# Performance work log

Hardware: AMD Instinct MI355X
Metric: run time of the kernel (lower is better)

## Reference

```python
import jax, jax.numpy as jnp
import numpy as np

N = 50000      # number of 'oa' nodes
E = 800000     # edges per metapath
IN_DIM = 128
OUT_DIM = 64   # per-head channels (concat=False -> mean over heads)
HEADS = 4
M = 3          # number of metapaths
NEG_SLOPE = 0.2  # PyG GATConv default leaky_relu slope


def setup_inputs() -> dict:
    key = jax.random.key(0)
    ks = jax.random.split(key, 32)
    inp = {"x": jax.random.normal(ks[0], (N, IN_DIM), jnp.float32)}
    for i in range(M):
        inp[f"edge_index_{i}"] = jax.random.randint(ks[1 + i], (2, E), 0, N, jnp.int32)
        inp[f"W_{i}"] = jax.random.normal(ks[4 + i], (IN_DIM, HEADS * OUT_DIM), jnp.float32) * (1.0 / np.sqrt(IN_DIM))
        inp[f"att_src_{i}"] = jax.random.normal(ks[7 + i], (HEADS, OUT_DIM), jnp.float32) * 0.1
        inp[f"att_dst_{i}"] = jax.random.normal(ks[10 + i], (HEADS, OUT_DIM), jnp.float32) * 0.1
        inp[f"bias_{i}"] = jnp.zeros((OUT_DIM,), jnp.float32)
    inp["proj_W"] = jax.random.normal(ks[20], (OUT_DIM, OUT_DIM), jnp.float32) * (1.0 / np.sqrt(OUT_DIM))
    inp["proj_b"] = jnp.zeros((OUT_DIM,), jnp.float32)
    inp["attn_vec"] = jax.random.normal(ks[21], (OUT_DIM,), jnp.float32) * 0.1
    return inp


def _gat_conv(x, edge_index, W, att_src, att_dst, bias):
    """PyG GATConv(in,out,heads,concat=False), eval mode, add_self_loops=True."""
    loop = jnp.arange(N, dtype=edge_index.dtype)
    src = jnp.concatenate([edge_index[0], loop])  # [E+N]
    dst = jnp.concatenate([edge_index[1], loop])
    h = (x @ W).reshape(N, HEADS, OUT_DIM)                 # [N,H,C]
    a_src = jnp.einsum('nhc,hc->nh', h, att_src)           # [N,H]
    a_dst = jnp.einsum('nhc,hc->nh', h, att_dst)
    e = jax.nn.leaky_relu(a_src[src] + a_dst[dst], NEG_SLOPE)  # [E+N,H]
    # edge softmax over incoming edges of each dst node (numerically stable)
    emax = jax.ops.segment_max(e, dst, num_segments=N)
    e = jnp.exp(e - emax[dst])
    denom = jax.ops.segment_sum(e, dst, num_segments=N)
    alpha = e / denom[dst]                                 # [E+N,H]; denom>0 via self loops
    out = jax.ops.segment_sum(h[src] * alpha[:, :, None], dst, num_segments=N)  # [N,H,C]
    return out.mean(axis=1) + bias                         # concat=False -> head mean


def reference(x, edge_index_0, edge_index_1, edge_index_2,
              W_0, W_1, W_2, att_src_0, att_src_1, att_src_2,
              att_dst_0, att_dst_1, att_dst_2, bias_0, bias_1, bias_2,
              proj_W, proj_b, attn_vec):
    eis = (edge_index_0, edge_index_1, edge_index_2)
    Ws = (W_0, W_1, W_2)
    a_s = (att_src_0, att_src_1, att_src_2)
    a_d = (att_dst_0, att_dst_1, att_dst_2)
    bs = (bias_0, bias_1, bias_2)
    z = [jax.nn.elu(_gat_conv(x, eis[i], Ws[i], a_s[i], a_d[i], bs[i])) for i in range(M)]
    z_stack = jnp.stack(z, axis=1)                          # [N,M,C]
    weights = jnp.tanh(z_stack @ proj_W + proj_b)           # [N,M,C]
    scores = jnp.einsum('nmc,c->nm', weights, attn_vec)     # [N,M]
    beta = jax.nn.softmax(scores, axis=1)                   # [N,M]
    z_final = jnp.einsum('nmc,nm->nc', z_stack, beta)       # [N,C]
    return z_final, beta
```

## Files before the change

kernel.cpp:

```cpp
#include <hip/hip_runtime.h>
#include <hip/hip_bf16.h>
#include <math.h>

#define NN 50000
#define EE 800000
#define IND 128
#define OUTD 64
#define NH 4
#define HC 256
#define WSZ 224
#define NWN 224
#define WCAP 4096
#define BATCH 2048
#define NBATCH ((EE + BATCH - 1) / BATCH)
#define PB (3 * NBATCH)
#define CVTB 6250
#define WPB 48
#define SORTB (3 * NWN)
#define NMT2 1563
#define MGB 391

typedef unsigned short u16;
typedef __attribute__((ext_vector_type(8))) short short8v;
typedef __attribute__((ext_vector_type(4))) float f32x4;
typedef __attribute__((ext_vector_type(2))) _Float16 half2v;

__device__ __forceinline__ float lrelu(float v) { return v > 0.f ? v : 0.2f * v; }
__device__ __forceinline__ u16 f2b(float f) {
  __hip_bfloat16 h = __float2bfloat16(f);
  return __builtin_bit_cast(u16, h);
}
__device__ __forceinline__ float b2f(u16 u) {
  return __uint_as_float((unsigned)u << 16);
}
__device__ __forceinline__ u16 f2h(float f) {
  _Float16 h = (_Float16)f;
  return __builtin_bit_cast(u16, h);
}
__device__ __forceinline__ float h2f(u16 u) {
  return (float)__builtin_bit_cast(_Float16, u);
}
__device__ __forceinline__ unsigned packh2(float a, float b) {
  half2v v = {(_Float16)a, (_Float16)b};
  return __builtin_bit_cast(unsigned, v);
}
__device__ __forceinline__ float dot2h(unsigned hpair, unsigned apair, float acc) {
#if __has_builtin(__builtin_amdgcn_fdot2)
  return __builtin_amdgcn_fdot2(__builtin_bit_cast(half2v, hpair),
                                __builtin_bit_cast(half2v, apair), acc, false);
#else
  acc = fmaf(h2f((u16)(hpair & 0xffff)), h2f((u16)(apair & 0xffff)), acc);
  return fmaf(h2f((u16)(hpair >> 16)), h2f((u16)(apair >> 16)), acc);
#endif
}

__global__ __launch_bounds__(256) void k_front(const int* __restrict__ ei0,
                                               const int* __restrict__ ei1,
                                               const int* __restrict__ ei2,
                                               int* __restrict__ gcur,
                                               unsigned int* __restrict__ glist,
                                               const float* __restrict__ x,
                                               u16* __restrict__ hi,
                                               u16* __restrict__ lo,
                                               const float* __restrict__ W0,
                                               const float* __restrict__ W1,
                                               const float* __restrict__ W2,
                                               const float* __restrict__ as0,
                                               const float* __restrict__ as1,
                                               const float* __restrict__ as2,
                                               const float* __restrict__ ad0,
                                               const float* __restrict__ ad1,
                                               const float* __restrict__ ad2,
                                               u16* __restrict__ wt,
                                               float* __restrict__ attS,
                                               float* __restrict__ attD) {
  __shared__ unsigned int stage[BATCH];
  __shared__ int cnt[NWN], strt[NWN], gbase[NWN];
  const int bx = blockIdx.x;
  const int tid = threadIdx.x;
  if (bx < PB) {
    const int m = bx / NBATCH;
    const int e0 = (bx - m * NBATCH) * BATCH;
    const int* ei = m == 0 ? ei0 : (m == 1 ? ei1 : ei2);
    if (tid < NWN) cnt[tid] = 0;
    __syncthreads();
    int bk[8], rk[8];
    unsigned int pk[8];
#pragma unroll
    for (int k = 0; k < 8; ++k) {
      const int e = e0 + k * 256 + tid;
      bk[k] = -1; rk[k] = 0; pk[k] = 0;
      if (e < EE) {
        const int d = ei[EE + e];
        const int s = ei[e];
        const int b = d / WSZ;
        bk[k] = b;
        pk[k] = ((unsigned)d << 16) | (unsigned)s;
        rk[k] = atomicAdd(&cnt[b], 1);
      }
    }
    __syncthreads();
    if (tid < 64) {
      const int base = tid * 4;
      int c0 = 0, c1 = 0, c2 = 0, c3 = 0;
      if (base + 0 < NWN) c0 = cnt[base + 0];
      if (base + 1 < NWN) c1 = cnt[base + 1];
      if (base + 2 < NWN) c2 = cnt[base + 2];
      if (base + 3 < NWN) c3 = cnt[base + 3];
      const int tot = c0 + c1 + c2 + c3;
      int run = tot;
#pragma unroll
      for (int off = 1; off < 64; off <<= 1) {
        const int u = __shfl_up(run, off, 64);
        if (tid >= off) run += u;
      }
      int ex = run - tot;
      if (base + 0 < NWN) { strt[base + 0] = ex; ex += c0; }
      if (base + 1 < NWN) { strt[base + 1] = ex; ex += c1; }
      if (base + 2 < NWN) { strt[base + 2] = ex; ex += c2; }
      if (base + 3 < NWN) { strt[base + 3] = ex; }
    }
    __syncthreads();
    if (tid < NWN && cnt[tid] > 0)
      gbase[tid] = atomicAdd(&gcur[m * NWN + tid], cnt[tid]);
#pragma unroll
    for (int k = 0; k < 8; ++k)
      if (bk[k] >= 0) stage[strt[bk[k]] + rk[k]] = pk[k];
    __syncthreads();
    const int unit = tid >> 3;
    const int l8 = tid & 7;
    for (int b = unit; b < NWN; b += 32) {
      const int len = cnt[b];
      if (len == 0) continue;
      const int st = strt[b];
      const int gb = gbase[b];
      unsigned int* dst = glist + (size_t)(m * NWN + b) * WCAP;
      for (int i = l8; i < len; i += 8)
        if (gb + i < WCAP) dst[gb + i] = stage[st + i];
    }
    return;
  }
  const int px = bx - PB;
  if (px < CVTB) {
    const int i = (px * 256 + tid) * 4;
    const float4 v = *(const float4*)(x + i);
    ushort4 h, l;
    h.x = f2b(v.x); l.x = f2b(v.x - b2f(h.x));
    h.y = f2b(v.y); l.y = f2b(v.y - b2f(h.y));
    h.z = f2b(v.z); l.z = f2b(v.z - b2f(h.z));
    h.w = f2b(v.w); l.w = f2b(v.w - b2f(h.w));
    *(ushort4*)(hi + i) = h;
    *(ushort4*)(lo + i) = l;
    return;
  }
  const int b = px - CVTB;
  const int m = b >> 4;
  const int kc = b & 15;
  const float* W = m == 0 ? W0 : (m == 1 ? W1 : W2);
  const int col = tid;
  const int colp = (col & 63) * 4 + (col >> 6);
#pragma unroll
  for (int kk = 0; kk < 8; ++kk) {
    const int k = kc * 8 + kk;
    wt[(size_t)m * (HC * IND) + colp * IND + k] = f2b(W[k * HC + col]);
  }
  if (kc == 0) {
    const float* as = m == 0 ? as0 : (m == 1 ? as1 : as2);
    const float* ad = m == 0 ? ad0 : (m == 1 ? ad1 : ad2);
    attS[m * HC + colp] = as[col];
    attD[m * HC + colp] = ad[col];
  }
}

__global__ __launch_bounds__(256) void k_mid(unsigned int* glist,
                                             const int* __restrict__ gcur,
                                             int* __restrict__ rowptr,
                                             const u16* __restrict__ xhi,
                                             const u16* __restrict__ xlo,
                                             const u16* __restrict__ wtB,
                                             const float* __restrict__ attSB,
                                             const float* __restrict__ attDB,
                                             u16* __restrict__ H16B,
                                             float* __restrict__ a_srcB,
                                             float* __restrict__ a_dstB,
                                             int nsort, int mbase,
                                             int strideH, int strideA) {
  __shared__ u16 srt[WCAP];
  __shared__ int cnt[WSZ], row[WSZ + 1], cur[WSZ];
  const int bx = blockIdx.x;
  const int tid = threadIdx.x;
  if (bx < nsort) {
    const int m = bx / NWN;
    const int w = bx - m * NWN;
    const int ne = min(gcur[m * NWN + w], WCAP);
    unsigned int* gl = glist + (size_t)(m * NWN + w) * WCAP;
    if (tid < WSZ) cnt[tid] = 0;
    __syncthreads();
    for (int i = tid; i < ne; i += 256)
      atomicAdd(&cnt[(int)(gl[i] >> 16) - w * WSZ], 1);
    __syncthreads();
    if (tid < 64) {
      const int base = tid * 4;
      int c0 = 0, c1 = 0, c2 = 0, c3 = 0;
      if (base + 0 < WSZ) c0 = cnt[base + 0];
      if (base + 1 < WSZ) c1 = cnt[base + 1];
      if (base + 2 < WSZ) c2 = cnt[base + 2];
      if (base + 3 < WSZ) c3 = cnt[base + 3];
      const int tot = c0 + c1 + c2 + c3;
      int run = tot;
#pragma unroll
      for (int off = 1; off < 64; off <<= 1) {
        const int u = __shfl_up(run, off, 64);
        if (tid >= off) run += u;
      }
      int ex = run - tot;
      if (base + 0 < WSZ) { row[base + 0] = ex; cur[base + 0] = ex; ex += c0; }
      if (base + 1 < WSZ) { row[base + 1] = ex; cur[base + 1] = ex; ex += c1; }
      if (base + 2 < WSZ) { row[base + 2] = ex; cur[base + 2] = ex; ex += c2; }
      if (base + 3 < WSZ) { row[base + 3] = ex; cur[base + 3] = ex; }
      if (tid == 63) row[WSZ] = ne;
    }
    __syncthreads();
    for (int i = tid; i < ne; i += 256) {
      const unsigned int v = gl[i];
      const int dl = (int)(v >> 16) - w * WSZ;
      const int p = atomicAdd(&cur[dl], 1);
      srt[p] = (u16)(v & 0xffffu);
    }
    __syncthreads();
    u16* cdst = (u16*)gl;
    for (int i = tid; i < ne; i += 256) cdst[i] = srt[i];
    int* rp = rowptr + (size_t)(m * NWN + w) * (WSZ + 1);
    if (tid <= WSZ) rp[tid] = row[tid];
    return;
  }
  const int b2 = bx - nsort;
  const int m = mbase + b2 / MGB;
  const int tg = b2 - (b2 / MGB) * MGB;
  const int wid = tid >> 6;
  const int l = tid & 63;
  const int l15 = l & 15;
  const int lq = l >> 4;
  const int mt = tg * 4 + wid;
  if (mt >= NMT2) return;
  const int m0 = mt * 32;
  const bool up = (m0 + 16 < NN);
  const u16* wt = wtB + (size_t)(m - mbase) * 0 + (size_t)m * (HC * IND);
  const float* attS = attSB + m * HC;
  const float* attD = attDB + m * HC;
  u16* H16 = H16B + (size_t)(m - mbase) * strideH;
  float* a_src = a_srcB + (size_t)(m - mbase) * strideA;
  float* a_dst = a_dstB + (size_t)(m - mbase) * strideA;
  const size_t aA = (size_t)(m0 + l15) * IND + lq * 8;
  const size_t aB = aA + (size_t)16 * IND;
  const u16* pb = wt + l15 * IND + lq * 8;
  f32x4 accA[16], accB[16];
#pragma unroll
  for (int nt = 0; nt < 16; ++nt) {
    accA[nt] = (f32x4){0.f, 0.f, 0.f, 0.f};
    accB[nt] = (f32x4){0.f, 0.f, 0.f, 0.f};
  }
#pragma unroll
  for (int ks = 0; ks < 4; ++ks) {
    const short8v a0h = *(const short8v*)(xhi + aA + ks * 32);
    const short8v a0l = *(const short8v*)(xlo + aA + ks * 32);
    short8v a1h = (short8v){0,0,0,0,0,0,0,0};
    short8v a1l = (short8v){0,0,0,0,0,0,0,0};
    if (up) {
      a1h = *(const short8v*)(xhi + aB + ks * 32);
      a1l = *(const short8v*)(xlo + aB + ks * 32);
    }
#pragma unroll
    for (int nt = 0; nt < 16; ++nt) {
      const short8v b0 = *(const short8v*)(pb + nt * 16 * IND + ks * 32);
      accA[nt] = __builtin_amdgcn_mfma_f32_16x16x32_bf16(a0h, b0, accA[nt], 0, 0, 0);
      accA[nt] = __builtin_amdgcn_mfma_f32_16x16x32_bf16(a0l, b0, accA[nt], 0, 0, 0);
      accB[nt] = __builtin_amdgcn_mfma_f32_16x16x32_bf16(a1h, b0, accB[nt], 0, 0, 0);
      accB[nt] = __builtin_amdgcn_mfma_f32_16x16x32_bf16(a1l, b0, accB[nt], 0, 0, 0);
    }
  }
#pragma unroll
  for (int nt = 0; nt < 16; ++nt) {
#pragma unroll
    for (int r = 0; r < 4; ++r)
      H16[(size_t)(m0 + lq * 4 + r) * HC + nt * 16 + l15] = f2h(accA[nt][r]);
  }
  if (up) {
#pragma unroll
    for (int nt = 0; nt < 16; ++nt) {
#pragma unroll
      for (int r = 0; r < 4; ++r)
        H16[(size_t)(m0 + 16 + lq * 4 + r) * HC + nt * 16 + l15] = f2h(accB[nt][r]);
    }
  }
  float asv[16], adv[16];
#pragma unroll
  for (int nt = 0; nt < 16; ++nt) {
    asv[nt] = attS[nt * 16 + l15];
    adv[nt] = attD[nt * 16 + l15];
  }
#pragma unroll
  for (int r = 0; r < 4; ++r) {
    float ps = 0.f, pd = 0.f, ps2 = 0.f, pd2 = 0.f;
#pragma unroll
    for (int nt = 0; nt < 16; ++nt) {
      ps = fmaf(accA[nt][r], asv[nt], ps);
      pd = fmaf(accA[nt][r], adv[nt], pd);
      ps2 = fmaf(accB[nt][r], asv[nt], ps2);
      pd2 = fmaf(accB[nt][r], adv[nt], pd2);
    }
    ps += __shfl_xor(ps, 4, 64); ps += __shfl_xor(ps, 8, 64);
    pd += __shfl_xor(pd, 4, 64); pd += __shfl_xor(pd, 8, 64);
    ps2 += __shfl_xor(ps2, 4, 64); ps2 += __shfl_xor(ps2, 8, 64);
    pd2 += __shfl_xor(pd2, 4, 64); pd2 += __shfl_xor(pd2, 8, 64);
    if (l15 < 4) {
      const int n = m0 + lq * 4 + r;
      a_src[n * NH + l15] = ps;
      a_dst[n * NH + l15] = pd;
      if (up) {
        a_src[(n + 16) * NH + l15] = ps2;
        a_dst[(n + 16) * NH + l15] = pd2;
      }
    }
  }
}

__global__ __launch_bounds__(256) void k_aggr(const unsigned int* __restrict__ glistB,
                                              const int* __restrict__ rowptrB,
                                              const u16* __restrict__ H16B,
                                              const float* __restrict__ a_srcB,
                                              const float* __restrict__ a_dstB,
                                              const float* __restrict__ b0_,
                                              const float* __restrict__ b1_,
                                              const float* __restrict__ b2_,
                                              u16* __restrict__ zbB,
                                              int mbase, int strideH, int strideA) {
  __shared__ uint4 slot[4][64];
  const int m = mbase + blockIdx.y;
  const unsigned int* glist_m = glistB + (size_t)m * NWN * WCAP;
  const int* rowptrm = rowptrB + (size_t)m * NWN * (WSZ + 1);
  const u16* H16 = H16B + (size_t)blockIdx.y * strideH;
  const float* a_src = a_srcB + (size_t)blockIdx.y * strideA;
  const float* a_dst = a_dstB + (size_t)blockIdx.y * strideA;
  const float* bias = m == 0 ? b0_ : (m == 1 ? b1_ : b2_);
  u16* zb = zbB + (size_t)m * NN * OUTD;
  const int wid = threadIdx.x >> 6;
  const int c = threadIdx.x & 63;
  const int d = blockIdx.x * 4 + wid;
  const int w = d / WSZ;
  const int dl = d - w * WSZ;
  const int* rp = rowptrm + (size_t)w * (WSZ + 1);
  const int r0 = rp[dl];
  const int nb = min(rp[dl + 1] - r0, 64);
  const u16* cw = (const u16*)(glist_m + (size_t)w * WCAP);
  const float4 adv = *(const float4*)&a_dst[d * NH];
  float4 evr = make_float4(0.f, 0.f, 0.f, 0.f);
  int sj = 0;
  if (c < nb) {
    sj = cw[r0 + c];
    const float4 asv = *(const float4*)&a_src[sj * NH];
    evr.x = __expf(lrelu(asv.x + adv.x));
    evr.y = __expf(lrelu(asv.y + adv.y));
    evr.z = __expf(lrelu(asv.z + adv.z));
    evr.w = __expf(lrelu(asv.w + adv.w));
  }
  float den0 = evr.x, den1 = evr.y, den2 = evr.z, den3 = evr.w;
#pragma unroll
  for (int mk = 32; mk; mk >>= 1) {
    den0 += __shfl_xor(den0, mk, 64);
    den1 += __shfl_xor(den1, mk, 64);
    den2 += __shfl_xor(den2, mk, 64);
    den3 += __shfl_xor(den3, mk, 64);
  }
  const float4 asl = *(const float4*)&a_src[d * NH];
  const float e0s = __expf(lrelu(asl.x + adv.x));
  const float e1s = __expf(lrelu(asl.y + adv.y));
  const float e2s = __expf(lrelu(asl.z + adv.z));
  const float e3s = __expf(lrelu(asl.w + adv.w));
  den0 += e0s; den1 += e1s; den2 += e2s; den3 += e3s;
  const float rd0 = 0.25f * __builtin_amdgcn_rcpf(den0);
  const float rd1 = 0.25f * __builtin_amdgcn_rcpf(den1);
  const float rd2 = 0.25f * __builtin_amdgcn_rcpf(den2);
  const float rd3 = 0.25f * __builtin_amdgcn_rcpf(den3);
  if (c < nb) {
    uint4 sv;
    sv.x = packh2(evr.x * rd0, evr.y * rd1);
    sv.y = packh2(evr.z * rd2, evr.w * rd3);
    sv.z = (unsigned)(sj * (HC * 2));
    sv.w = 0;
    slot[wid][c] = sv;
  }
  const ushort4 hs = *(const ushort4*)&H16[(size_t)d * HC + c * 4];
  float res = e0s * rd0 * h2f(hs.x);
  res = fmaf(e1s * rd1, h2f(hs.y), res);
  res = fmaf(e2s * rd2, h2f(hs.z), res);
  res = fmaf(e3s * rd3, h2f(hs.w), res);
  const unsigned char* Hb = (const unsigned char*)H16;
  const int c8 = c * 8;
  float accA = 0.f, accB = 0.f, accC = 0.f, accD = 0.f;
  int j = 0;
  for (; j + 4 <= nb; j += 4) {
    const uint4 sa = slot[wid][j + 0];
    const uint4 sb = slot[wid][j + 1];
    const uint4 sc = slot[wid][j + 2];
    const uint4 sd = slot[wid][j + 3];
    const uint2 ha = *(const uint2*)(Hb + (size_t)sa.z + c8);
    const uint2 hb = *(const uint2*)(Hb + (size_t)sb.z + c8);
    const uint2 hc = *(const uint2*)(Hb + (size_t)sc.z + c8);
    const uint2 hd = *(const uint2*)(Hb + (size_t)sd.z + c8);
    accA = dot2h(ha.x, sa.x, accA); accA = dot2h(ha.y, sa.y, accA);
    accB = dot2h(hb.x, sb.x, accB); accB = dot2h(hb.y, sb.y, accB);
    accC = dot2h(hc.x, sc.x, accC); accC = dot2h(hc.y, sc.y, accC);
    accD = dot2h(hd.x, sd.x, accD); accD = dot2h(hd.y, sd.y, accD);
  }
  for (; j < nb; ++j) {
    const uint4 sa = slot[wid][j];
    const uint2 ha = *(const uint2*)(Hb + (size_t)sa.z + c8);
    accA = dot2h(ha.x, sa.x, accA);
    accA = dot2h(ha.y, sa.y, accA);
  }
  res += (accA + accB) + (accC + accD);
  res += bias[c];
  res = res > 0.f ? res : __expf(res) - 1.f;
  zb[(size_t)d * OUTD + c] = f2b(res);
}

__global__ __launch_bounds__(256) void k_sem(const u16* __restrict__ zb,
                                             const float* __restrict__ proj_W,
                                             const float* __restrict__ proj_b,
                                             const float* __restrict__ attn_vec,
                                             float* __restrict__ out) {
  __shared__ float zl[3][16][OUTD];
  const int tid = threadIdx.x;
  const int n0 = blockIdx.x * 16;
  const int wid = tid >> 6;
  const int c = tid & 63;
  float pwc[64];
#pragma unroll
  for (int k = 0; k < 64; ++k) pwc[k] = proj_W[k * OUTD + c];
#pragma unroll
  for (int mm = 0; mm < 3; ++mm) {
    const ushort4 v = ((const ushort4*)(zb + ((size_t)mm * NN + n0) * OUTD))[tid];
    float4 f;
    f.x = b2f(v.x); f.y = b2f(v.y); f.z = b2f(v.z); f.w = b2f(v.w);
    *(float4*)&zl[mm][tid >> 4][(tid & 15) * 4] = f;
  }
  __syncthreads();
  const float pb = proj_b[c];
  const float av = attn_vec[c];
  for (int nl = 0; nl < 4; ++nl) {
    const int node = wid * 4 + nl;
    float s[3];
#pragma unroll
    for (int mm = 0; mm < 3; ++mm) {
      const float4* zr = (const float4*)&zl[mm][node][0];
      float a0 = pb, a1 = 0.f, a2 = 0.f, a3 = 0.f;
#pragma unroll
      for (int kq = 0; kq < 4; ++kq) {
        const float4 z0 = zr[kq * 4 + 0];
        const float4 z1 = zr[kq * 4 + 1];
        const float4 z2 = zr[kq * 4 + 2];
        const float4 z3 = zr[kq * 4 + 3];
        a0 = fmaf(z0.x, pwc[kq * 16 + 0], a0);
        a0 = fmaf(z0.y, pwc[kq * 16 + 1], a0);
        a0 = fmaf(z0.z, pwc[kq * 16 + 2], a0);
        a0 = fmaf(z0.w, pwc[kq * 16 + 3], a0);
        a1 = fmaf(z1.x, pwc[kq * 16 + 4], a1);
        a1 = fmaf(z1.y, pwc[kq * 16 + 5], a1);
        a1 = fmaf(z1.z, pwc[kq * 16 + 6], a1);
        a1 = fmaf(z1.w, pwc[kq * 16 + 7], a1);
        a2 = fmaf(z2.x, pwc[kq * 16 + 8], a2);
        a2 = fmaf(z2.y, pwc[kq * 16 + 9], a2);
        a2 = fmaf(z2.z, pwc[kq * 16 + 10], a2);
        a2 = fmaf(z2.w, pwc[kq * 16 + 11], a2);
        a3 = fmaf(z3.x, pwc[kq * 16 + 12], a3);
        a3 = fmaf(z3.y, pwc[kq * 16 + 13], a3);
        a3 = fmaf(z3.z, pwc[kq * 16 + 14], a3);
        a3 = fmaf(z3.w, pwc[kq * 16 + 15], a3);
      }
      float xx = (a0 + a1) + (a2 + a3);
      xx = fminf(xx, 40.f);
      const float t = __expf(2.f * xx);
      const float th = (t - 1.f) * __builtin_amdgcn_rcpf(t + 1.f);
      float p = th * av;
#pragma unroll
      for (int mk = 32; mk; mk >>= 1) p += __shfl_xor(p, mk, 64);
      s[mm] = p;
    }
    const float mx = fmaxf(s[0], fmaxf(s[1], s[2]));
    const float e0 = __expf(s[0] - mx), e1 = __expf(s[1] - mx), e2 = __expf(s[2] - mx);
    const float inv = 1.0f / (e0 + e1 + e2);
    const float b0 = e0 * inv, b1 = e1 * inv, b2 = e2 * inv;
    const int n = n0 + node;
    const float zf = zl[0][node][c] * b0 + zl[1][node][c] * b1 + zl[2][node][c] * b2;
    out[(size_t)n * OUTD + c] = zf;
    if (c < 3) out[(size_t)NN * OUTD + n * 3 + c] = (c == 0 ? b0 : (c == 1 ? b1 : b2));
  }
}

extern "C" void kernel_launch(void* const* d_in, const int* in_sizes, int n_in,
                              void* d_out, int out_size, void* d_ws, size_t ws_size,
                              hipStream_t stream) {
  const float* x = (const float*)d_in[0];
  const int* ei[3];
  const float* W[3];
  const float* as[3];
  const float* ad[3];
  const float* bs[3];

  if (in_sizes[2] != 2 * EE) {
    for (int m = 0; m < 3; ++m) {
      ei[m] = (const int*)d_in[1 + 5 * m];
      W[m]  = (const float*)d_in[2 + 5 * m];
      as[m] = (const float*)d_in[3 + 5 * m];
      ad[m] = (const float*)d_in[4 + 5 * m];
      bs[m] = (const float*)d_in[5 + 5 * m];
    }
  } else {
    for (int m = 0; m < 3; ++m) {
      ei[m] = (const int*)d_in[1 + m];
      W[m]  = (const float*)d_in[4 + m];
      as[m] = (const float*)d_in[7 + m];
      ad[m] = (const float*)d_in[10 + m];
      bs[m] = (const float*)d_in[13 + m];
    }
  }
  const float* proj_W = (const float*)d_in[16];
  const float* proj_b = (const float*)d_in[17];
  const float* attn_vec = (const float*)d_in[18];

  const bool batched = (ws_size >= (size_t)139000000);
  const int nrep = batched ? 3 : 1;

  char* ws = (char*)d_ws;
  size_t off = 0;
  u16* x16hi = (u16*)(ws + off);                     off += (size_t)NN * IND * 2;
  u16* x16lo = (u16*)(ws + off);                     off += (size_t)NN * IND * 2;
  u16* H16 = (u16*)(ws + off);                       off += (size_t)nrep * NN * HC * 2;
  u16* zb = (u16*)(ws + off);                        off += (size_t)3 * NN * OUTD * 2;
  float* a_srcb = (float*)(ws + off);                off += (size_t)nrep * NN * NH * 4;
  float* a_dstb = (float*)(ws + off);                off += (size_t)nrep * NN * NH * 4;
  int* gcur = (int*)(ws + off);                      off += (size_t)3 * NWN * 4;
  unsigned int* glist = (unsigned int*)(ws + off);   off += (size_t)3 * NWN * WCAP * 4;
  int* rowptr = (int*)(ws + off);                    off += (size_t)3 * NWN * (WSZ + 1) * 4;
  u16* wt16 = (u16*)(ws + off);                      off += (size_t)3 * HC * IND * 2;
  float* attSp = (float*)(ws + off);                 off += (size_t)3 * HC * 4;
  float* attDp = (float*)(ws + off);                 off += (size_t)3 * HC * 4;

  float* outp = (float*)d_out;

  hipMemsetAsync(gcur, 0, (size_t)3 * NWN * sizeof(int), stream);
  k_front<<<PB + CVTB + WPB, 256, 0, stream>>>(ei[0], ei[1], ei[2], gcur, glist,
                                               x, x16hi, x16lo,
                                               W[0], W[1], W[2], as[0], as[1], as[2],
                                               ad[0], ad[1], ad[2], wt16, attSp, attDp);

  if (batched) {
    k_mid<<<SORTB + 3 * MGB, 256, 0, stream>>>(glist, gcur, rowptr,
                                               x16hi, x16lo, wt16, attSp, attDp,
                                               H16, a_srcb, a_dstb,
                                               SORTB, 0, NN * HC, NN * NH);
    k_aggr<<<dim3(NN / 4, 3), 256, 0, stream>>>(
        glist, rowptr, H16, a_srcb, a_dstb, bs[0], bs[1], bs[2], zb,
        0, NN * HC, NN * NH);
  } else {
    k_mid<<<SORTB + MGB, 256, 0, stream>>>(glist, gcur, rowptr,
                                           x16hi, x16lo, wt16, attSp, attDp,
                                           H16, a_srcb, a_dstb,
                                           SORTB, 0, 0, 0);
    k_aggr<<<dim3(NN / 4, 1), 256, 0, stream>>>(
        glist, rowptr, H16, a_srcb, a_dstb, bs[0], bs[1], bs[2], zb, 0, 0, 0);
    for (int m = 1; m < 3; ++m) {
      k_mid<<<MGB, 256, 0, stream>>>(glist, gcur, rowptr,
                                     x16hi, x16lo, wt16, attSp, attDp,
                                     H16, a_srcb, a_dstb,
                                     0, m, 0, 0);
      k_aggr<<<dim3(NN / 4, 1), 256, 0, stream>>>(
          glist, rowptr, H16, a_srcb, a_dstb, bs[0], bs[1], bs[2], zb, m, 0, 0);
    }
  }
  k_sem<<<NN / 16, 256, 0, stream>>>(zb, proj_W, proj_b, attn_vec, outp);
}
```

Baseline: 320.1 us.

## Fuse x bf16 split into GEMM, loop metapaths per wave, double edge batch

The separate pass that split x into bf16 hi/lo arrays in the front kernel is removed. The GEMM kernel now reads fp32 x directly, converts it in registers once, and reuses those fragments across all metapaths. Each wave now handles a 16-row tile and loops over the 3 metapaths instead of a 32-row tile for one metapath, which cuts x reads and the hi/lo workspace traffic. The edge binning batch size is also doubled to 4096 per block, giving fewer blocks and fewer global atomics at the cost of more registers. Lowering the workspace threshold lets the batched path run with less memory, and the metapath loop serialises the GEMM work within each wave.

```diff
diff --git a/kernel.cpp b/kernel.cpp
--- a/kernel.cpp
+++ b/kernel.cpp
@@ -11,14 +11,13 @@
 #define WSZ 224
 #define NWN 224
 #define WCAP 4096
-#define BATCH 2048
+#define BATCH 4096
 #define NBATCH ((EE + BATCH - 1) / BATCH)
 #define PB (3 * NBATCH)
-#define CVTB 6250
 #define WPB 48
 #define SORTB (3 * NWN)
-#define NMT2 1563
-#define MGB 391
+#define NMT 3125
+#define MG3B ((NMT + 3) / 4)
 
 typedef unsigned short u16;
 typedef __attribute__((ext_vector_type(8))) short short8v;
@@ -59,9 +58,6 @@
                                                const int* __restrict__ ei2,
                                                int* __restrict__ gcur,
                                                unsigned int* __restrict__ glist,
-                                               const float* __restrict__ x,
-                                               u16* __restrict__ hi,
-                                               u16* __restrict__ lo,
                                                const float* __restrict__ W0,
                                                const float* __restrict__ W1,
                                                const float* __restrict__ W2,
@@ -84,10 +80,10 @@
     const int* ei = m == 0 ? ei0 : (m == 1 ? ei1 : ei2);
     if (tid < NWN) cnt[tid] = 0;
     __syncthreads();
-    int bk[8], rk[8];
-    unsigned int pk[8];
-#pragma unroll
-    for (int k = 0; k < 8; ++k) {
+    int bk[16], rk[16];
+    unsigned int pk[16];
+#pragma unroll
+    for (int k = 0; k < 16; ++k) {
       const int e = e0 + k * 256 + tid;
       bk[k] = -1; rk[k] = 0; pk[k] = 0;
       if (e < EE) {
@@ -124,7 +120,7 @@
     if (tid < NWN && cnt[tid] > 0)
       gbase[tid] = atomicAdd(&gcur[m * NWN + tid], cnt[tid]);
 #pragma unroll
-    for (int k = 0; k < 8; ++k)
+    for (int k = 0; k < 16; ++k)
       if (bk[k] >= 0) stage[strt[bk[k]] + rk[k]] = pk[k];
     __syncthreads();
     const int unit = tid >> 3;
@@ -140,20 +136,7 @@
     }
     return;
   }
-  const int px = bx - PB;
-  if (px < CVTB) {
-    const int i = (px * 256 + tid) * 4;
-    const float4 v = *(const float4*)(x + i);
-    ushort4 h, l;
-    h.x = f2b(v.x); l.x = f2b(v.x - b2f(h.x));
-    h.y = f2b(v.y); l.y = f2b(v.y - b2f(h.y));
-    h.z = f2b(v.z); l.z = f2b(v.z - b2f(h.z));
-    h.w = f2b(v.w); l.w = f2b(v.w - b2f(h.w));
-    *(ushort4*)(hi + i) = h;
-    *(ushort4*)(lo + i) = l;
-    return;
-  }
-  const int b = px - CVTB;
+  const int b = bx - PB;
   const int m = b >> 4;
   const int kc = b & 15;
   const float* W = m == 0 ? W0 : (m == 1 ? W1 : W2);
@@ -175,15 +158,14 @@
 __global__ __launch_bounds__(256) void k_mid(unsigned int* glist,
                                              const int* __restrict__ gcur,
                                              int* __restrict__ rowptr,
-                                             const u16* __restrict__ xhi,
-                                             const u16* __restrict__ xlo,
+                                             const float* __restrict__ x,
                                              const u16* __restrict__ wtB,
                                              const float* __restrict__ attSB,
                                              const float* __restrict__ attDB,
                                              u16* __restrict__ H16B,
                                              float* __restrict__ a_srcB,
                                              float* __restrict__ a_dstB,
-                                             int nsort, int mbase,
+                                             int nsort, int mg_base, int mg_count,
                                              int strideH, int strideA) {
   __shared__ u16 srt[WCAP];
   __shared__ int cnt[WSZ], row[WSZ + 1], cur[WSZ];
@@ -235,91 +217,77 @@
     return;
   }
   const int b2 = bx - nsort;
-  const int m = mbase + b2 / MGB;
-  const int tg = b2 - (b2 / MGB) * MGB;
   const int wid = tid >> 6;
   const int l = tid & 63;
   const int l15 = l & 15;
   const int lq = l >> 4;
-  const int mt = tg * 4 + wid;
-  if (mt >= NMT2) return;
-  const int m0 = mt * 32;
-  const bool up = (m0 + 16 < NN);
-  const u16* wt = wtB + (size_t)(m - mbase) * 0 + (size_t)m * (HC * IND);
-  const float* attS = attSB + m * HC;
-  const float* attD = attDB + m * HC;
-  u16* H16 = H16B + (size_t)(m - mbase) * strideH;
-  float* a_src = a_srcB + (size_t)(m - mbase) * strideA;
-  float* a_dst = a_dstB + (size_t)(m - mbase) * strideA;
-  const size_t aA = (size_t)(m0 + l15) * IND + lq * 8;
-  const size_t aB = aA + (size_t)16 * IND;
-  const u16* pb = wt + l15 * IND + lq * 8;
-  f32x4 accA[16], accB[16];
-#pragma unroll
-  for (int nt = 0; nt < 16; ++nt) {
-    accA[nt] = (f32x4){0.f, 0.f, 0.f, 0.f};
-    accB[nt] = (f32x4){0.f, 0.f, 0.f, 0.f};
-  }
+  const int mt = b2 * 4 + wid;
+  if (mt >= NMT) return;
+  const int m0 = mt * 16;
+  const float* px = x + (size_t)(m0 + l15) * IND + lq * 8;
+  short8v ah[4], al[4];
 #pragma unroll
   for (int ks = 0; ks < 4; ++ks) {
-    const short8v a0h = *(const short8v*)(xhi + aA + ks * 32);
-    const short8v a0l = *(const short8v*)(xlo + aA + ks * 32);
-    short8v a1h = (short8v){0,0,0,0,0,0,0,0};
-    short8v a1l = (short8v){0,0,0,0,0,0,0,0};
-    if (up) {
-      a1h = *(const short8v*)(xhi + aB + ks * 32);
-      a1l = *(const short8v*)(xlo + aB + ks * 32);
-    }
+    const float4 f0 = *(const float4*)(px + ks * 32);
+    const float4 f1 = *(const float4*)(px + ks * 32 + 4);
+    short8v h, lo;
+    const u16 h0 = f2b(f0.x); h[0] = (short)h0; lo[0] = (short)f2b(f0.x - b2f(h0));
+    const u16 h1 = f2b(f0.y); h[1] = (short)h1; lo[1] = (short)f2b(f0.y - b2f(h1));
+    const u16 h2 = f2b(f0.z); h[2] = (short)h2; lo[2] = (short)f2b(f0.z - b2f(h2));
+    const u16 h3 = f2b(f0.w); h[3] = (short)h3; lo[3] = (short)f2b(f0.w - b2f(h3));
+    const u16 h4 = f2b(f1.x); h[4] = (short)h4; lo[4] = (short)f2b(f1.x - b2f(h4));
+    const u16 h5 = f2b(f1.y); h[5] = (short)h5; lo[5] = (short)f2b(f1.y - b2f(h5));
+    const u16 h6 = f2b(f1.z); h[6] = (short)h6; lo[6] = (short)f2b(f1.z - b2f(h6));
+    const u16 h7 = f2b(f1.w); h[7] = (short)h7; lo[7] = (short)f2b(f1.w - b2f(h7));
+    ah[ks] = h;
+    al[ks] = lo;
+  }
+  for (int mm = 0; mm < mg_count; ++mm) {
+    const int m = mg_base + mm;
+    const u16* pb = wtB + (size_t)m * (HC * IND) + l15 * IND + lq * 8;
+    f32x4 acc[16];
+#pragma unroll
+    for (int nt = 0; nt < 16; ++nt) acc[nt] = (f32x4){0.f, 0.f, 0.f, 0.f};
+#pragma unroll
+    for (int ks = 0; ks < 4; ++ks) {
+#pragma unroll
+      for (int nt = 0; nt < 16; ++nt) {
+        const short8v b0 = *(const short8v*)(pb + nt * 16 * IND + ks * 32);
+        acc[nt] = __builtin_amdgcn_mfma_f32_16x16x32_bf16(ah[ks], b0, acc[nt], 0, 0, 0);
+        acc[nt] = __builtin_amdgcn_mfma_f32_16x16x32_bf16(al[ks], b0, acc[nt], 0, 0, 0);
+      }
+    }
+    u16* H16 = H16B + (size_t)mm * strideH;
 #pragma unroll
     for (int nt = 0; nt < 16; ++nt) {
-      const short8v b0 = *(const short8v*)(pb + nt * 16 * IND + ks * 32);
-      accA[nt] = __builtin_amdgcn_mfma_f32_16x16x32_bf16(a0h, b0, accA[nt], 0, 0, 0);
-      accA[nt] = __builtin_amdgcn_mfma_f32_16x16x32_bf16(a0l, b0, accA[nt], 0, 0, 0);
-      accB[nt] = __builtin_amdgcn_mfma_f32_16x16x32_bf16(a1h, b0, accB[nt], 0, 0, 0);
-      accB[nt] = __builtin_amdgcn_mfma_f32_16x16x32_bf16(a1l, b0, accB[nt], 0, 0, 0);
-    }
-  }
-#pragma unroll
-  for (int nt = 0; nt < 16; ++nt) {
-#pragma unroll
-    for (int r = 0; r < 4; ++r)
-      H16[(size_t)(m0 + lq * 4 + r) * HC + nt * 16 + l15] = f2h(accA[nt][r]);
-  }
-  if (up) {
+#pragma unroll
+      for (int r = 0; r < 4; ++r)
+        H16[(size_t)(m0 + lq * 4 + r) * HC + nt * 16 + l15] = f2h(acc[nt][r]);
+    }
+    const float* attS = attSB + m * HC;
+    const float* attD = attDB + m * HC;
+    float asv[16], adv[16];
 #pragma unroll
     for (int nt = 0; nt < 16; ++nt) {
-#pragma unroll
-      for (int r = 0; r < 4; ++r)
-        H16[(size_t)(m0 + 16 + lq * 4 + r) * HC + nt * 16 + l15] = f2h(accB[nt][r]);
-    }
-  }
-  float asv[16], adv[16];
-#pragma unroll
-  for (int nt = 0; nt < 16; ++nt) {
-    asv[nt] = attS[nt * 16 + l15];
-    adv[nt] = attD[nt * 16 + l15];
-  }
-#pragma unroll
-  for (int r = 0; r < 4; ++r) {
-    float ps = 0.f, pd = 0.f, ps2 = 0.f, pd2 = 0.f;
-#pragma unroll
-    for (int nt = 0; nt < 16; ++nt) {
-      ps = fmaf(accA[nt][r], asv[nt], ps);
-      pd = fmaf(accA[nt][r], adv[nt], pd);
-      ps2 = fmaf(accB[nt][r], asv[nt], ps2);
-      pd2 = fmaf(accB[nt][r], adv[nt], pd2);
-    }
-    ps += __shfl_xor(ps, 4, 64); ps += __shfl_xor(ps, 8, 64);
-    pd += __shfl_xor(pd, 4, 64); pd += __shfl_xor(pd, 8, 64);
-    ps2 += __shfl_xor(ps2, 4, 64); ps2 += __shfl_xor(ps2, 8, 64);
-    pd2 += __shfl_xor(pd2, 4, 64); pd2 += __shfl_xor(pd2, 8, 64);
-    if (l15 < 4) {
-      const int n = m0 + lq * 4 + r;
-      a_src[n * NH + l15] = ps;
-      a_dst[n * NH + l15] = pd;
-      if (up) {
-        a_src[(n + 16) * NH + l15] = ps2;
-        a_dst[(n + 16) * NH + l15] = pd2;
+      asv[nt] = attS[nt * 16 + l15];
+      adv[nt] = attD[nt * 16 + l15];
+    }
+    float* a_src = a_srcB + (size_t)mm * strideA;
+    float* a_dst = a_dstB + (size_t)mm * strideA;
+#pragma unroll
+    for (int r = 0; r < 4; ++r) {
+      float ps = 0.f, pd = 0.f;
+#pragma unroll
+      for (int nt = 0; nt < 16; ++nt) {
+        ps = fmaf(acc[nt][r], asv[nt], ps);
+        pd = fmaf(acc[nt][r], adv[nt], pd);
+      }
+      ps += __shfl_xor(ps, 4, 64); ps += __shfl_xor(ps, 8, 64);
+      pd += __shfl_xor(pd, 4, 64); pd += __shfl_xor(pd, 8, 64);
+      if (l15 < 4) {
+        const int n = m0 + lq * 4 + r;
+        a_src[n * NH + l15] = ps;
+        a_dst[n * NH + l15] = pd;
       }
     }
   }
@@ -529,13 +497,11 @@
   const float* proj_b = (const float*)d_in[17];
   const float* attn_vec = (const float*)d_in[18];
 
-  const bool batched = (ws_size >= (size_t)139000000);
+  const bool batched = (ws_size >= (size_t)115000000);
   const int nrep = batched ? 3 : 1;
 
   char* ws = (char*)d_ws;
   size_t off = 0;
-  u16* x16hi = (u16*)(ws + off);                     off += (size_t)NN * IND * 2;
-  u16* x16lo = (u16*)(ws + off);                     off += (size_t)NN * IND * 2;
   u16* H16 = (u16*)(ws + off);                       off += (size_t)nrep * NN * HC * 2;
   u16* zb = (u16*)(ws + off);                        off += (size_t)3 * NN * OUTD * 2;
   float* a_srcb = (float*)(ws + off);                off += (size_t)nrep * NN * NH * 4;
@@ -550,31 +516,30 @@
   float* outp = (float*)d_out;
 
   hipMemsetAsync(gcur, 0, (size_t)3 * NWN * sizeof(int), stream);
-  k_front<<<PB + CVTB + WPB, 256, 0, stream>>>(ei[0], ei[1], ei[2], gcur, glist,
-                                               x, x16hi, x16lo,
-                                               W[0], W[1], W[2], as[0], as[1], as[2],
-                                               ad[0], ad[1], ad[2], wt16, attSp, attDp);
+  k_front<<<PB + WPB, 256, 0, stream>>>(ei[0], ei[1], ei[2], gcur, glist,
+                                        W[0], W[1], W[2], as[0], as[1], as[2],
+                                        ad[0], ad[1], ad[2], wt16, attSp, attDp);
 
   if (batched) {
-    k_mid<<<SORTB + 3 * MGB, 256, 0, stream>>>(glist, gcur, rowptr,
-                                               x16hi, x16lo, wt16, attSp, attDp,
-                                               H16, a_srcb, a_dstb,
-                                               SORTB, 0, NN * HC, NN * NH);
+    k_mid<<<SORTB + MG3B, 256, 0, stream>>>(glist, gcur, rowptr, x,
+                                            wt16, attSp, attDp,
+                                            H16, a_srcb, a_dstb,
+                                            SORTB, 0, 3, NN * HC, NN * NH);
     k_aggr<<<dim3(NN / 4, 3), 256, 0, stream>>>(
         glist, rowptr, H16, a_srcb, a_dstb, bs[0], bs[1], bs[2], zb,
         0, NN * HC, NN * NH);
   } else {
-    k_mid<<<SORTB + MGB, 256, 0, stream>>>(glist, gcur, rowptr,
-                                           x16hi, x16lo, wt16, attSp, attDp,
-                                           H16, a_srcb, a_dstb,
-                                           SORTB, 0, 0, 0);
+    k_mid<<<SORTB + MG3B, 256, 0, stream>>>(glist, gcur, rowptr, x,
+                                            wt16, attSp, attDp,
+                                            H16, a_srcb, a_dstb,
+                                            SORTB, 0, 1, 0, 0);
     k_aggr<<<dim3(NN / 4, 1), 256, 0, stream>>>(
         glist, rowptr, H16, a_srcb, a_dstb, bs[0], bs[1], bs[2], zb, 0, 0, 0);
     for (int m = 1; m < 3; ++m) {
-      k_mid<<<MGB, 256, 0, stream>>>(glist, gcur, rowptr,
-                                     x16hi, x16lo, wt16, attSp, attDp,
-                                     H16, a_srcb, a_dstb,
-                                     0, m, 0, 0);
+      k_mid<<<MG3B, 256, 0, stream>>>(glist, gcur, rowptr, x,
+                                      wt16, attSp, attDp,
+                                      H16, a_srcb, a_dstb,
+                                      0, m, 1, 0, 0);
       k_aggr<<<dim3(NN / 4, 1), 256, 0, stream>>>(
           glist, rowptr, H16, a_srcb, a_dstb, bs[0], bs[1], bs[2], zb, m, 0, 0);
     }
```

New measurement: 348.7 us. +8.9%, slower.
